# Performance work log

Hardware: AMD Instinct MI355X
Metric: run time of the kernel (lower is better)

Reference implementation:

```python
import jax, jax.numpy as jnp
import numpy as np

SRC_SIZE = 1024
TGT_SIZE = 1024
ATT_SIZE = 1024
S, T, B = 1024, 1024, 32


def setup_inputs() -> dict:
    key = jax.random.key(0)
    k1, k2, k3, k4 = jax.random.split(key, 4)
    source = jax.random.normal(k1, (S, B, SRC_SIZE), dtype=jnp.float32)
    target = jax.random.normal(k2, (T, B, TGT_SIZE), dtype=jnp.float32)
    # nn.Linear(in, out, bias=False): weight shape (out, in), y = x @ W.T
    scale1 = 1.0 / np.sqrt(SRC_SIZE)
    scale2 = 1.0 / np.sqrt(TGT_SIZE)
    W1 = jax.random.uniform(k3, (ATT_SIZE, SRC_SIZE), dtype=jnp.float32, minval=-scale1, maxval=scale1)
    W2 = jax.random.uniform(k4, (ATT_SIZE, TGT_SIZE), dtype=jnp.float32, minval=-scale2, maxval=scale2)
    return {"source": source, "target": target, "W1": W1, "W2": W2}


def reference(source, target, W1, W2):
    # Transform into attention space: (S,B,A) and (T,B,A)
    ts = jnp.einsum('sbd,ad->sba', source, W1)
    tt = jnp.einsum('tbd,ad->tba', target, W2)
    # Multiplicative scores: (S,T,B) = sum_a ts[s,b,a]*tt[t,b,a]
    scores = jnp.einsum('sba,tba->stb', ts, tt)
    # Softmax over source positions (axis 0)
    weights = jax.nn.softmax(scores, axis=0)  # (S,T,B)
    # Attention vectors: (T,B,src_size) = sum_s weights[s,t,b]*source[s,b,d]
    return jnp.einsum('stb,sbd->tbd', weights, source)
```

## Files before the change

kernel.cpp:

```cpp
#include <hip/hip_runtime.h>
#include <hip/hip_bf16.h>

typedef _Float16 half_t;
typedef __attribute__((ext_vector_type(8))) _Float16 half8;
typedef __attribute__((ext_vector_type(4))) _Float16 half4;
typedef __attribute__((ext_vector_type(4))) float floatx4;
typedef __attribute__((ext_vector_type(4))) float f32x4;

#define DEVFN static __device__ __forceinline__

DEVFN void gll16(const void* g, void* l) {
    __builtin_amdgcn_global_load_lds(
        (const __attribute__((address_space(1))) unsigned int*)g,
        (__attribute__((address_space(3))) unsigned int*)l, 16, 0, 0);
}
DEVFN f32x4 mfma16(half8 a, half8 b, f32x4 c) {
    return __builtin_amdgcn_mfma_f32_16x16x32_f16(a, b, c, 0, 0, 0);
}
DEVFN void lgkm0() { asm volatile("s_waitcnt lgkmcnt(0)" ::: "memory"); __builtin_amdgcn_sched_barrier(0); }
DEVFN void vm0()   { asm volatile("s_waitcnt vmcnt(0)"   ::: "memory"); __builtin_amdgcn_sched_barrier(0); }
DEVFN void vm2()   { asm volatile("s_waitcnt vmcnt(2)"   ::: "memory"); __builtin_amdgcn_sched_barrier(0); }
DEVFN void vm4()   { asm volatile("s_waitcnt vmcnt(4)"   ::: "memory"); __builtin_amdgcn_sched_barrier(0); }
DEVFN void bar()   { __builtin_amdgcn_s_barrier(); __builtin_amdgcn_sched_barrier(0); }

__global__ __launch_bounds__(256) void cvt_f16(
    const float* __restrict__ in, half_t* __restrict__ out, int n4)
{
    int i = blockIdx.x * 256 + threadIdx.x;
    if (i >= n4) return;
    floatx4 v = ((const floatx4*)in)[i];
    half4 h;
#pragma unroll
    for (int j = 0; j < 4; j++) h[j] = (half_t)v[j];
    ((half4*)out)[i] = h;
}

__global__ __launch_bounds__(256) void transpose_src_f16(
    const float* __restrict__ src, half_t* __restrict__ srcT, half_t* __restrict__ srcH)
{
    __shared__ float tile[32][33];
    int s0 = blockIdx.x << 5, d0 = blockIdx.y << 5, b = blockIdx.z;
    int t = threadIdx.x;
    int si = t >> 3, dj = (t & 7) << 2;
    floatx4 v = *(const floatx4*)&src[((size_t)(s0 + si) * 32 + b) * 1024 + d0 + dj];
    tile[si][dj + 0] = v[0]; tile[si][dj + 1] = v[1];
    tile[si][dj + 2] = v[2]; tile[si][dj + 3] = v[3];
    half4 hv;
#pragma unroll
    for (int j = 0; j < 4; j++) hv[j] = (half_t)v[j];
    *(half4*)&srcH[((size_t)(s0 + si) * 32 + b) * 1024 + d0 + dj] = hv;
    __syncthreads();
    int di = t >> 3, sj = (t & 7) << 2;
    half4 o;
#pragma unroll
    for (int q = 0; q < 4; q++) o[q] = (half_t)tile[sj + q][di];
    *(half4*)&srcT[((size_t)b * 1024 + d0 + di) * 1024 + s0 + sj] = o;
}

template <bool OUT_F16>
__global__ __launch_bounds__(512, 2) void gemm256(
    const half_t* __restrict__ A, const half_t* __restrict__ B,
    void* __restrict__ Cv,
    int lda, int ldb, int ldc, int K,
    long long bA, long long bB, long long bC,
    int gx, int gy)
{
    __shared__ char lds[131072];
    const int nwg = gridDim.x;
    const int bid = blockIdx.x;
    const int sw = (bid & 7) * (nwg >> 3) + (bid >> 3);
    const int x = sw % gx;
    const int r1 = sw / gx;
    const int y = r1 % gy;
    const int z = r1 / gy;

    const int t = threadIdx.x, lane = t & 63, w = t >> 6;
    const int wr = w >> 2, wc = w & 3;
    const int m0 = y << 8, n0 = x << 8;
    const half_t* pA = A + (size_t)bA * z + (size_t)m0 * lda;
    const half_t* pB = B + (size_t)bB * z + (size_t)n0 * ldb;

    int srow[2], scol[2];
#pragma unroll
    for (int i = 0; i < 2; i++) {
        int slot = (w << 7) + (i << 6) + lane;
        srow[i] = slot >> 2;
        scol[i] = (slot & 3) << 3;
    }
    const unsigned stOff = (unsigned)((w << 7) << 4);

    const int lr = lane & 15, q = lane >> 4;
    const unsigned aRd = (unsigned)((((wr << 7) + lr) << 6) + (q << 4));
    const unsigned bRd = 65536u + (unsigned)((((wc << 6) + lr) << 6) + (q << 4));

    f32x4 acc[8][4];
#pragma unroll
    for (int m = 0; m < 8; m++)
#pragma unroll
        for (int n = 0; n < 4; n++) acc[m][n] = (f32x4){0.f, 0.f, 0.f, 0.f};

    auto stA = [&](int nb, int kh, int kc) {
#pragma unroll
        for (int i = 0; i < 2; i++)
            gll16(pA + (size_t)srow[i] * lda + (kc + kh * 32 + scol[i]),
                  lds + (nb << 15) + (kh << 14) + stOff + (i << 10));
    };
    auto stB = [&](int nb, int kh, int kc) {
#pragma unroll
        for (int i = 0; i < 2; i++)
            gll16(pB + (size_t)srow[i] * ldb + (kc + kh * 32 + scol[i]),
                  lds + 65536 + (nb << 15) + (kh << 14) + stOff + (i << 10));
    };

    stA(0, 0, 0); stA(0, 1, 0); stB(0, 0, 0); stB(0, 1, 0);
    vm2();
    bar();

    half8 av[8], bv[2], bv2[2];
    const int NT = K >> 6;
    for (int tt = 0; tt < NT; ++tt) {
        const int buf = tt & 1, nb = buf ^ 1;
        const bool st = (tt + 1 < NT);
        const int kn = (tt + 1) << 6;
        const unsigned base0 = (unsigned)(buf << 15);
        const unsigned base1 = base0 + 16384u;

#pragma unroll
        for (int m = 0; m < 8; m++) av[m] = *(const half8*)(lds + base0 + aRd + m * 1024);
#pragma unroll
        for (int n = 0; n < 2; n++) bv[n] = *(const half8*)(lds + base0 + bRd + n * 1024);
        if (st) stA(nb, 0, kn);
        bar();
        lgkm0();
        __builtin_amdgcn_s_setprio(1);
#pragma unroll
        for (int m = 0; m < 8; m++) {
            acc[m][0] = mfma16(av[m], bv[0], acc[m][0]);
            acc[m][1] = mfma16(av[m], bv[1], acc[m][1]);
        }
        __builtin_amdgcn_s_setprio(0);
        bar();

#pragma unroll
        for (int n = 0; n < 2; n++) bv2[n] = *(const half8*)(lds + base0 + bRd + (2 + n) * 1024);
        if (st) stA(nb, 1, kn);
        bar();
        lgkm0();
        __builtin_amdgcn_s_setprio(1);
#pragma unroll
        for (int m = 0; m < 8; m++) {
            acc[m][2] = mfma16(av[m], bv2[0], acc[m][2]);
            acc[m][3] = mfma16(av[m], bv2[1], acc[m][3]);
        }
        __builtin_amdgcn_s_setprio(0);
        if (st) vm4(); else vm0();
        bar();

#pragma unroll
        for (int m = 0; m < 8; m++) av[m] = *(const half8*)(lds + base1 + aRd + m * 1024);
#pragma unroll
        for (int n = 0; n < 2; n++) bv[n] = *(const half8*)(lds + base1 + bRd + n * 1024);
        if (st) stB(nb, 0, kn);
        bar();
        lgkm0();
        __builtin_amdgcn_s_setprio(1);
#pragma unroll
        for (int m = 0; m < 8; m++) {
            acc[m][0] = mfma16(av[m], bv[0], acc[m][0]);
            acc[m][1] = mfma16(av[m], bv[1], acc[m][1]);
        }
        __builtin_amdgcn_s_setprio(0);
        bar();

#pragma unroll
        for (int n = 0; n < 2; n++) bv2[n] = *(const half8*)(lds + base1 + bRd + (2 + n) * 1024);
        if (st) stB(nb, 1, kn);
        bar();
        lgkm0();
        __builtin_amdgcn_s_setprio(1);
#pragma unroll
        for (int m = 0; m < 8; m++) {
            acc[m][2] = mfma16(av[m], bv2[0], acc[m][2]);
            acc[m][3] = mfma16(av[m], bv2[1], acc[m][3]);
        }
        __builtin_amdgcn_s_setprio(0);
        if (st) vm2();
        bar();
    }

    const size_t zC = (size_t)bC * z;
    const int r0 = m0 + (wr << 7) + (q << 2);
    const int c0 = n0 + (wc << 6) + lr;
#pragma unroll
    for (int m = 0; m < 8; m++)
#pragma unroll
        for (int fn = 0; fn < 4; fn++)
#pragma unroll
            for (int j = 0; j < 4; j++) {
                size_t idx = zC + (size_t)(r0 + m * 16 + j) * ldc + (c0 + fn * 16);
                if constexpr (OUT_F16)
                    ((half_t*)Cv)[idx] = (half_t)acc[m][fn][j];
                else
                    ((float*)Cv)[idx] = acc[m][fn][j];
            }
}

__global__ __launch_bounds__(256) void softmax_k(
    const float* __restrict__ sc, half_t* __restrict__ wt)
{
    size_t row = blockIdx.x;
    const floatx4* p = (const floatx4*)(sc + row * 1024);
    int t = threadIdx.x, lane = t & 63, w = t >> 6;
    floatx4 v = p[t];
    float m = fmaxf(fmaxf(v[0], v[1]), fmaxf(v[2], v[3]));
#pragma unroll
    for (int o = 1; o < 64; o <<= 1) m = fmaxf(m, __shfl_xor(m, o));
    __shared__ float red[8];
    if (lane == 0) red[w] = m;
    __syncthreads();
    m = fmaxf(fmaxf(red[0], red[1]), fmaxf(red[2], red[3]));
    floatx4 e;
#pragma unroll
    for (int j = 0; j < 4; j++) e[j] = __expf(v[j] - m);
    float s = e[0] + e[1] + e[2] + e[3];
#pragma unroll
    for (int o = 1; o < 64; o <<= 1) s += __shfl_xor(s, o);
    if (lane == 0) red[4 + w] = s;
    __syncthreads();
    s = red[4] + red[5] + red[6] + red[7];
    float inv = 1.0f / s;
    half4 o4;
#pragma unroll
    for (int j = 0; j < 4; j++) o4[j] = (half_t)(e[j] * inv);
    ((half4*)(wt + row * 1024))[t] = o4;
}

extern "C" void kernel_launch(void* const* d_in, const int* in_sizes, int n_in,
                              void* d_out, int out_size, void* d_ws, size_t ws_size,
                              hipStream_t stream)
{
    const float* src = (const float*)d_in[0];
    const float* tgt = (const float*)d_in[1];
    const float* W1  = (const float*)d_in[2];
    const float* W2  = (const float*)d_in[3];
    float* out = (float*)d_out;

    char* ws = (char*)d_ws;
    const size_t MB = 1024ull * 1024ull;
    half_t* srcH  = (half_t*)(ws);
    half_t* tgtH  = (half_t*)(ws + 64  * MB);
    half_t* tsH   = (half_t*)(ws + 128 * MB);
    half_t* ttH   = (half_t*)(ws + 192 * MB);
    half_t* srcT  = (half_t*)(ws + 256 * MB);
    float*  scores= (float*) (ws + 320 * MB);
    half_t* w1h   = (half_t*)(ws + 448 * MB);
    half_t* w2h   = (half_t*)(ws + 450 * MB);
    half_t* wts   = srcH;

    cvt_f16<<<32768, 256, 0, stream>>>(tgt, tgtH, 8388608);
    cvt_f16<<<1024, 256, 0, stream>>>(W1, w1h, 262144);
    cvt_f16<<<1024, 256, 0, stream>>>(W2, w2h, 262144);
    transpose_src_f16<<<dim3(32, 32, 32), 256, 0, stream>>>(src, srcT, srcH);

    gemm256<true><<<512, 512, 0, stream>>>(srcH, w1h, tsH,
        1024, 1024, 1024, 1024, 0ll, 0ll, 0ll, 4, 128);
    gemm256<true><<<512, 512, 0, stream>>>(tgtH, w2h, ttH,
        1024, 1024, 1024, 1024, 0ll, 0ll, 0ll, 4, 128);

    gemm256<false><<<512, 512, 0, stream>>>(ttH, tsH, scores,
        32768, 32768, 1024, 1024, 1024ll, 1024ll, 1024ll * 1024ll, 4, 4);

    softmax_k<<<32768, 256, 0, stream>>>(scores, wts);

    gemm256<false><<<512, 512, 0, stream>>>(wts, srcT, out,
        1024, 1024, 32768, 1024, 1024ll * 1024ll, 1024ll * 1024ll, 1024ll, 4, 4);
}
```

Measured before the change: 707.7 us.

## Reschedule GEMM main loop with fewer barriers and interleaved LDS loads

Rewrites the double-buffered MFMA main loop so each K-tile is split into four 4x4 MFMA quadrants, with LDS fragment loads for the next quadrant issued before the current quadrant's MFMAs. This cuts per-iteration barriers from eight to two and drops the explicit lgkmcnt waits, leaving LDS wait placement to the compiler. Global-to-LDS prefetches are spread between the MFMA groups and guarded by vmcnt(4) waits. The aim is less barrier stall and better overlap of LDS reads with MFMA work, at the cost of more live fragment registers and tighter reliance on correct wait counts.

Result: no change. 701.1 us (-0.9%).

```diff
diff --git a/kernel.cpp b/kernel.cpp
--- a/kernel.cpp
+++ b/kernel.cpp
@@ -17,11 +17,9 @@
 DEVFN f32x4 mfma16(half8 a, half8 b, f32x4 c) {
     return __builtin_amdgcn_mfma_f32_16x16x32_f16(a, b, c, 0, 0, 0);
 }
-DEVFN void lgkm0() { asm volatile("s_waitcnt lgkmcnt(0)" ::: "memory"); __builtin_amdgcn_sched_barrier(0); }
-DEVFN void vm0()   { asm volatile("s_waitcnt vmcnt(0)"   ::: "memory"); __builtin_amdgcn_sched_barrier(0); }
-DEVFN void vm2()   { asm volatile("s_waitcnt vmcnt(2)"   ::: "memory"); __builtin_amdgcn_sched_barrier(0); }
-DEVFN void vm4()   { asm volatile("s_waitcnt vmcnt(4)"   ::: "memory"); __builtin_amdgcn_sched_barrier(0); }
-DEVFN void bar()   { __builtin_amdgcn_s_barrier(); __builtin_amdgcn_sched_barrier(0); }
+DEVFN void vm0() { asm volatile("s_waitcnt vmcnt(0)" ::: "memory"); __builtin_amdgcn_sched_barrier(0); }
+DEVFN void vm4() { asm volatile("s_waitcnt vmcnt(4)" ::: "memory"); __builtin_amdgcn_sched_barrier(0); }
+DEVFN void bar() { __builtin_amdgcn_s_barrier(); __builtin_amdgcn_sched_barrier(0); }
 
 __global__ __launch_bounds__(256) void cvt_f16(
     const float* __restrict__ in, half_t* __restrict__ out, int n4)
@@ -112,80 +110,66 @@
                   lds + 65536 + (nb << 15) + (kh << 14) + stOff + (i << 10));
     };
 
-    stA(0, 0, 0); stA(0, 1, 0); stB(0, 0, 0); stB(0, 1, 0);
-    vm2();
-    bar();
-
-    half8 av[8], bv[2], bv2[2];
+    stA(0, 0, 0); stB(0, 0, 0); stA(0, 1, 0); stB(0, 1, 0);
+
+    half8 av_a[4], av_b[4], bv0[4], bv1[4];
     const int NT = K >> 6;
     for (int tt = 0; tt < NT; ++tt) {
         const int buf = tt & 1, nb = buf ^ 1;
         const bool st = (tt + 1 < NT);
         const int kn = (tt + 1) << 6;
-        const unsigned base0 = (unsigned)(buf << 15);
-        const unsigned base1 = base0 + 16384u;
-
-#pragma unroll
-        for (int m = 0; m < 8; m++) av[m] = *(const half8*)(lds + base0 + aRd + m * 1024);
-#pragma unroll
-        for (int n = 0; n < 2; n++) bv[n] = *(const half8*)(lds + base0 + bRd + n * 1024);
+        const unsigned b0 = (unsigned)(buf << 15);
+        const unsigned b1 = b0 + 16384u;
+
+        vm4();
+        bar();
         if (st) stA(nb, 0, kn);
-        bar();
-        lgkm0();
-        __builtin_amdgcn_s_setprio(1);
-#pragma unroll
-        for (int m = 0; m < 8; m++) {
-            acc[m][0] = mfma16(av[m], bv[0], acc[m][0]);
-            acc[m][1] = mfma16(av[m], bv[1], acc[m][1]);
-        }
-        __builtin_amdgcn_s_setprio(0);
-        bar();
-
-#pragma unroll
-        for (int n = 0; n < 2; n++) bv2[n] = *(const half8*)(lds + base0 + bRd + (2 + n) * 1024);
-        if (st) stA(nb, 1, kn);
-        bar();
-        lgkm0();
-        __builtin_amdgcn_s_setprio(1);
-#pragma unroll
-        for (int m = 0; m < 8; m++) {
-            acc[m][2] = mfma16(av[m], bv2[0], acc[m][2]);
-            acc[m][3] = mfma16(av[m], bv2[1], acc[m][3]);
-        }
-        __builtin_amdgcn_s_setprio(0);
+#pragma unroll
+        for (int m = 0; m < 4; m++) av_a[m] = *(const half8*)(lds + b0 + aRd + m * 1024);
+#pragma unroll
+        for (int n = 0; n < 4; n++) bv0[n] = *(const half8*)(lds + b0 + bRd + n * 1024);
+#pragma unroll
+        for (int m = 0; m < 4; m++) av_b[m] = *(const half8*)(lds + b0 + aRd + (4 + m) * 1024);
+        __builtin_amdgcn_s_setprio(1);
+#pragma unroll
+        for (int m = 0; m < 4; m++)
+#pragma unroll
+            for (int n = 0; n < 4; n++)
+                acc[m][n] = mfma16(av_a[m], bv0[n], acc[m][n]);
+        __builtin_amdgcn_s_setprio(0);
+        if (st) stB(nb, 0, kn);
+
         if (st) vm4(); else vm0();
         bar();
-
-#pragma unroll
-        for (int m = 0; m < 8; m++) av[m] = *(const half8*)(lds + base1 + aRd + m * 1024);
-#pragma unroll
-        for (int n = 0; n < 2; n++) bv[n] = *(const half8*)(lds + base1 + bRd + n * 1024);
-        if (st) stB(nb, 0, kn);
-        bar();
-        lgkm0();
-        __builtin_amdgcn_s_setprio(1);
-#pragma unroll
-        for (int m = 0; m < 8; m++) {
-            acc[m][0] = mfma16(av[m], bv[0], acc[m][0]);
-            acc[m][1] = mfma16(av[m], bv[1], acc[m][1]);
-        }
-        __builtin_amdgcn_s_setprio(0);
-        bar();
-
-#pragma unroll
-        for (int n = 0; n < 2; n++) bv2[n] = *(const half8*)(lds + base1 + bRd + (2 + n) * 1024);
+#pragma unroll
+        for (int m = 0; m < 4; m++) av_a[m] = *(const half8*)(lds + b1 + aRd + m * 1024);
+#pragma unroll
+        for (int n = 0; n < 4; n++) bv1[n] = *(const half8*)(lds + b1 + bRd + n * 1024);
+        __builtin_amdgcn_s_setprio(1);
+#pragma unroll
+        for (int m = 0; m < 4; m++)
+#pragma unroll
+            for (int n = 0; n < 4; n++)
+                acc[4 + m][n] = mfma16(av_b[m], bv0[n], acc[4 + m][n]);
+        __builtin_amdgcn_s_setprio(0);
+        if (st) stA(nb, 1, kn);
+#pragma unroll
+        for (int m = 0; m < 4; m++) av_b[m] = *(const half8*)(lds + b1 + aRd + (4 + m) * 1024);
+        __builtin_amdgcn_s_setprio(1);
+#pragma unroll
+        for (int m = 0; m < 4; m++)
+#pragma unroll
+            for (int n = 0; n < 4; n++)
+                acc[m][n] = mfma16(av_a[m], bv1[n], acc[m][n]);
+        __builtin_amdgcn_s_setprio(0);
         if (st) stB(nb, 1, kn);
-        bar();
-        lgkm0();
-        __builtin_amdgcn_s_setprio(1);
-#pragma unroll
-        for (int m = 0; m < 8; m++) {
-            acc[m][2] = mfma16(av[m], bv2[0], acc[m][2]);
-            acc[m][3] = mfma16(av[m], bv2[1], acc[m][3]);
-        }
-        __builtin_amdgcn_s_setprio(0);
-        if (st) vm2();
-        bar();
+        __builtin_amdgcn_s_setprio(1);
+#pragma unroll
+        for (int m = 0; m < 4; m++)
+#pragma unroll
+            for (int n = 0; n < 4; n++)
+                acc[4 + m][n] = mfma16(av_b[m], bv1[n], acc[4 + m][n]);
+        __builtin_amdgcn_s_setprio(0);
     }
 
     const size_t zC = (size_t)bC * z;
```
